# Kernel tuning notes

Hardware: AMD Instinct MI355X
Metric: run time of the kernel (lower is better)

Reference implementation:

```python
import jax, jax.numpy as jnp
import numpy as np

UNITS = 1024
INPUT_DIM = 2048
OUTPUT_DIM = 1000
EPS = 0.01
DT = 0.1
BATCH = 8192


def _kaiming_like(key, shape, fan_in):
    # matches torch kaiming_uniform_(a=sqrt(5)) bound = sqrt(6/((1+5)*fan_in)) = 1/sqrt(fan_in)
    bound = 1.0 / np.sqrt(fan_in)
    return jax.random.uniform(key, shape, jnp.float32, -bound, bound)


def setup_inputs() -> dict:
    key = jax.random.key(0)
    ks = jax.random.split(key, 12)
    x = jax.random.normal(ks[0], (BATCH, INPUT_DIM), jnp.float32)
    W_in = _kaiming_like(ks[1], (UNITS, INPUT_DIM), INPUT_DIM)
    b_in = _kaiming_like(ks[2], (UNITS,), INPUT_DIM)
    W1 = _kaiming_like(ks[3], (UNITS, UNITS), UNITS)
    b1 = _kaiming_like(ks[4], (UNITS,), UNITS)
    W2 = _kaiming_like(ks[5], (UNITS, UNITS), UNITS)
    b2 = _kaiming_like(ks[6], (UNITS,), UNITS)
    W3 = _kaiming_like(ks[7], (UNITS, UNITS), UNITS)
    b3 = _kaiming_like(ks[8], (UNITS,), UNITS)
    W_out = _kaiming_like(ks[9], (OUTPUT_DIM, UNITS), UNITS)
    b_out = _kaiming_like(ks[10], (OUTPUT_DIM,), UNITS)
    return {"x": x, "W_in": W_in, "b_in": b_in, "W1": W1, "b1": b1,
            "W2": W2, "b2": b2, "W3": W3, "b3": b3,
            "W_out": W_out, "b_out": b_out}


def transnet_layer(z, W, b):
    # z: (B, 2U). Implicit layer: A y = rhs, output = C y - rhs (== -y mathematically)
    U = W.shape[0]
    u_in, v_in = z[:, :U], z[:, U:]
    relu_u = jax.nn.relu(u_in)
    rhs_u = u_in + DT * b                      # (B, U)
    rhs_v = v_in + (DT / EPS) * relu_u         # (B, U)
    rhs = jnp.concatenate([rhs_u, rhs_v], axis=1)  # (B, 2U)
    eye = jnp.eye(U, dtype=z.dtype)
    A = jnp.block([[eye, DT * W],
                   [-DT * W.T, (1.0 + DT / EPS) * eye]])  # (2U, 2U), batch-independent
    # factor once, solve against all batch rhs columns at once
    y = jnp.linalg.solve(A, rhs.T).T           # (B, 2U)
    u, v = y[:, :U], y[:, U:]
    u_out = DT * (v @ W.T) - u_in - DT * b
    v_out = -DT * (u @ W) + (DT / EPS) * v - v_in - (DT / EPS) * relu_u
    return jnp.concatenate([u_out, v_out], axis=1)


def reference(x, W_in, b_in, W1, b1, W2, b2, W3, b3, W_out, b_out):
    z = x @ W_in.T + b_in                      # (B, U)
    z = jnp.concatenate([z, jax.nn.relu(z)], axis=1)  # (B, 2U)
    z = transnet_layer(z, W1, b1)
    z = transnet_layer(z, W2, b2)
    z = transnet_layer(z, W3, b3)
    z = z[:, :UNITS]
    logits = jax.nn.softmax(z @ W_out.T + b_out, axis=1)
    return logits
```

## Files before the change

kernel.cpp:

```cpp
#include <hip/hip_runtime.h>
#include <hip/hip_bf16.h>
#include <cstdint>


typedef __bf16 bf16;
typedef __bf16 bf16x4 __attribute__((ext_vector_type(4)));
typedef __bf16 bf16x8 __attribute__((ext_vector_type(8)));
typedef float  f32x4  __attribute__((ext_vector_type(4)));

#define C_DT    0.1f
#define C_DTEPS 10.0f
#define C_DINV  (1.0f/11.0f)
#define C_MSC   (0.01f/121.0f)

__device__ __forceinline__ void async_load16(const bf16* g, bf16* l) {
    __builtin_amdgcn_global_load_lds(
        (__attribute__((address_space(1))) void*)(g),
        (__attribute__((address_space(3))) void*)(l),
        16, 0, 0);
}

__device__ __forceinline__ void remap_block(int& bx, int& by) {
    if (gridDim.y == 64) {
        const int lin  = by * 8 + bx;
        const int xcd  = lin & 7;
        const int slot = lin >> 3;
        by = xcd * 8 + (slot & 7);
        bx = slot >> 3;
    }
}

template<int EPI>
__global__ __launch_bounds__(256, 2)
void gemm_bt(const bf16* __restrict__ A, const bf16* __restrict__ B,
             float* __restrict__ out_f,
             bf16* __restrict__ out_b1, bf16* __restrict__ out_b2,
             const float* __restrict__ e0, const float* __restrict__ e1,
             const float* __restrict__ e2, const bf16* __restrict__ eb,
             int M, int N, int K, float sgn)
{
    __shared__ __attribute__((aligned(16))) char smem[16384];
    bf16* sA = (bf16*)smem;
    bf16* sB = (bf16*)(smem + 8192);

    const int t    = threadIdx.x;
    const int wave = t >> 6;
    const int lane = t & 63;
    int bx = blockIdx.x, by = blockIdx.y;
    remap_block(bx, by);
    const long row0 = (long)by * 128;
    const long col0 = (long)bx * 128;
    const int wr = wave >> 1, wc = wave & 1;

    f32x4 acc[4][4];
#pragma unroll
    for (int i = 0; i < 4; i++)
#pragma unroll
        for (int j = 0; j < 4; j++)
            acc[i][j] = f32x4{0.f, 0.f, 0.f, 0.f};

    const int  q  = t >> 2;
    const int  gp = ((t & 3) + 4 - ((q + (q >> 2)) & 3)) & 3;
    const int  scol = gp * 8;
    const bf16* gA = A + (row0 + q) * (long)K + scol;
    const bf16* gB = B + (col0 + q) * (long)K + scol;
    bf16* lA = sA + wave * 512;
    bf16* lB = sB + wave * 512;

    const int l15  = lane & 15;
    const int fch  = ((lane >> 4) + l15 + (l15 >> 2)) & 3;
    const int aoff = (wr * 64 + l15) * 32 + fch * 8;
    const int boff = (wc * 64 + l15) * 32 + fch * 8;

    for (int k0 = 0; k0 < K; k0 += 32) {
        __syncthreads();
        async_load16(gA + k0,                 lA);
        async_load16(gA + 64 * (long)K + k0,  lA + 2048);
        async_load16(gB + k0,                 lB);
        async_load16(gB + 64 * (long)K + k0,  lB + 2048);
        __syncthreads();

        bf16x8 af[4], bfv[4];
#pragma unroll
        for (int i = 0; i < 4; i++)
            af[i] = *(const bf16x8*)(sA + aoff + i * 16 * 32);
#pragma unroll
        for (int j = 0; j < 4; j++)
            bfv[j] = *(const bf16x8*)(sB + boff + j * 16 * 32);
#pragma unroll
        for (int i = 0; i < 4; i++)
#pragma unroll
            for (int j = 0; j < 4; j++)
                acc[i][j] = __builtin_amdgcn_mfma_f32_16x16x32_bf16(
                    af[i], bfv[j], acc[i][j], 0, 0, 0);
    }

    __syncthreads();
    float* epi = (float*)smem + wave * 1024;
    const int wbase = (lane >> 4) * 256 + (l15 >> 2) * 4 + (l15 & 3);

#pragma unroll
    for (int i = 0; i < 4; i++) {
#pragma unroll
        for (int j = 0; j < 4; j++)
#pragma unroll
            for (int r = 0; r < 4; r++)
                epi[wbase + r * 64 + 16 * j] = acc[i][j][r];

#pragma unroll
        for (int qq = 0; qq < 4; qq++) {
            const f32x4 a4 = ((const f32x4*)epi)[qq * 64 + lane];
            const long m   = row0 + wr * 64 + i * 16 + qq * 4 + (lane >> 4);
            const long n   = col0 + wc * 64 + 4 * l15;
            const long idx = m * (long)N + n;

            if (EPI == 0) {
                const f32x4 b0 = *(const f32x4*)(e0 + n);
                const f32x4 b1 = *(const f32x4*)(e1 + n);
                f32x4 tv; bf16x4 rv, hv;
#pragma unroll
                for (int e = 0; e < 4; e++) {
                    tv[e] = a4[e] + b0[e];
                    rv[e] = (bf16)fmaxf(tv[e], 0.f);
                    hv[e] = (bf16)(tv[e] + C_DT * b1[e]);
                }
                *(f32x4*)(out_f + idx)   = tv;
                *(bf16x4*)(out_b1 + idx) = rv;
                *(bf16x4*)(out_b2 + idx) = hv;
            } else if (EPI == 1) {
                bf16x4 ov;
#pragma unroll
                for (int e = 0; e < 4; e++)
                    ov[e] = (bf16)(((m == n + e) ? C_DINV : 0.f) - C_MSC * a4[e]);
                *(bf16x4*)(out_b1 + idx) = ov;
            } else if (EPI == 2) {
                const f32x4  u0 = *(const f32x4*)(e0 + idx);
                const bf16x4 vv = *(const bf16x4*)(eb + idx);
                bf16x4 ov;
#pragma unroll
                for (int e = 0; e < 4; e++)
                    ov[e] = (bf16)(sgn * (float)vv[e]
                                   + C_DTEPS * fmaxf(u0[e], 0.f) + C_DT * a4[e]);
                *(bf16x4*)(out_b1 + idx) = ov;
            } else if (EPI == 3) {
                bf16x4 ov;
#pragma unroll
                for (int e = 0; e < 4; e++) ov[e] = (bf16)a4[e];
                *(bf16x4*)(out_b1 + idx) = ov;
            } else if (EPI == 4) {
                const f32x4 u0 = *(const f32x4*)(e0 + idx);
                const f32x4 b1 = *(const f32x4*)(e1 + n);
                const f32x4 b2 = *(const f32x4*)(e2 + n);
                f32x4 un; bf16x4 hv;
#pragma unroll
                for (int e = 0; e < 4; e++) {
                    un[e] = C_DT * a4[e] - u0[e] - C_DT * b1[e];
                    hv[e] = (bf16)(un[e] + C_DT * b2[e]);
                }
                *(f32x4*)(out_f + idx)   = un;
                *(bf16x4*)(out_b1 + idx) = hv;
            } else {
                const f32x4 u0 = *(const f32x4*)(e0 + idx);
                const f32x4 b1 = *(const f32x4*)(e1 + n);
                bf16x4 hv, lv;
#pragma unroll
                for (int e = 0; e < 4; e++) {
                    float un = C_DT * a4[e] - u0[e] - C_DT * b1[e];
                    bf16 h = (bf16)un;
                    hv[e] = h;
                    lv[e] = (bf16)(un - (float)h);
                }
                *(bf16x4*)(out_b1 + idx) = hv;
                *(bf16x4*)(out_b2 + idx) = lv;
            }
        }
    }
}

__global__ __launch_bounds__(256, 2)
void gemm_split(const bf16* __restrict__ Ah, const bf16* __restrict__ Al,
                const bf16* __restrict__ Bh, const bf16* __restrict__ Bl,
                float* __restrict__ out, const float* __restrict__ bias,
                int M, int N, int K, int blim)
{
    __shared__ __attribute__((aligned(16))) char smem[32768];
    bf16* sAh = (bf16*)smem;
    bf16* sAl = (bf16*)(smem +  8192);
    bf16* sBh = (bf16*)(smem + 16384);
    bf16* sBl = (bf16*)(smem + 24576);

    const int t    = threadIdx.x;
    const int wave = t >> 6;
    const int lane = t & 63;
    int bx = blockIdx.x, by = blockIdx.y;
    remap_block(bx, by);
    const long row0 = (long)by * 128;
    const long col0 = (long)bx * 128;
    const int wr = wave >> 1, wc = wave & 1;

    f32x4 acc[4][4];
#pragma unroll
    for (int i = 0; i < 4; i++)
#pragma unroll
        for (int j = 0; j < 4; j++)
            acc[i][j] = f32x4{0.f, 0.f, 0.f, 0.f};

    const int  q  = t >> 2;
    const int  gp = ((t & 3) + 4 - ((q + (q >> 2)) & 3)) & 3;
    const int  scol = gp * 8;
    const long gao = (row0 + q) * (long)K + scol;
    const long gbo = (col0 + q) * (long)K + scol;
    const int  lo  = wave * 512;

    const int l15  = lane & 15;
    const int fch  = ((lane >> 4) + l15 + (l15 >> 2)) & 3;
    const int aoff = (wr * 64 + l15) * 32 + fch * 8;
    const int boff = (wc * 64 + l15) * 32 + fch * 8;

    for (int k0 = 0; k0 < K; k0 += 32) {
        __syncthreads();
        async_load16(Ah + gao + k0,                 sAh + lo);
        async_load16(Ah + gao + 64 * (long)K + k0,  sAh + lo + 2048);
        async_load16(Al + gao + k0,                 sAl + lo);
        async_load16(Al + gao + 64 * (long)K + k0,  sAl + lo + 2048);
        async_load16(Bh + gbo + k0,                 sBh + lo);
        async_load16(Bh + gbo + 64 * (long)K + k0,  sBh + lo + 2048);
        async_load16(Bl + gbo + k0,                 sBl + lo);
        async_load16(Bl + gbo + 64 * (long)K + k0,  sBl + lo + 2048);
        __syncthreads();

        bf16x8 ah[4], al[4], bh[4], bl[4];
#pragma unroll
        for (int i = 0; i < 4; i++) {
            ah[i] = *(const bf16x8*)(sAh + aoff + i * 16 * 32);
            al[i] = *(const bf16x8*)(sAl + aoff + i * 16 * 32);
        }
#pragma unroll
        for (int j = 0; j < 4; j++) {
            bh[j] = *(const bf16x8*)(sBh + boff + j * 16 * 32);
            bl[j] = *(const bf16x8*)(sBl + boff + j * 16 * 32);
        }
#pragma unroll
        for (int i = 0; i < 4; i++)
#pragma unroll
            for (int j = 0; j < 4; j++) {
                acc[i][j] = __builtin_amdgcn_mfma_f32_16x16x32_bf16(
                    ah[i], bh[j], acc[i][j], 0, 0, 0);
                acc[i][j] = __builtin_amdgcn_mfma_f32_16x16x32_bf16(
                    ah[i], bl[j], acc[i][j], 0, 0, 0);
                acc[i][j] = __builtin_amdgcn_mfma_f32_16x16x32_bf16(
                    al[i], bh[j], acc[i][j], 0, 0, 0);
            }
    }

    __syncthreads();
    float* epi = (float*)smem + wave * 1024;
    const int wbase = (lane >> 4) * 256 + (l15 >> 2) * 4 + (l15 & 3);

#pragma unroll
    for (int i = 0; i < 4; i++) {
#pragma unroll
        for (int j = 0; j < 4; j++)
#pragma unroll
            for (int r = 0; r < 4; r++)
                epi[wbase + r * 64 + 16 * j] = acc[i][j][r];

#pragma unroll
        for (int qq = 0; qq < 4; qq++) {
            f32x4 a4 = ((const f32x4*)epi)[qq * 64 + lane];
            const long m   = row0 + wr * 64 + i * 16 + qq * 4 + (lane >> 4);
            const long n   = col0 + wc * 64 + 4 * l15;
            f32x4 bv = f32x4{0.f, 0.f, 0.f, 0.f};
            if (n < blim) bv = *(const f32x4*)(bias + n);
#pragma unroll
            for (int e = 0; e < 4; e++) a4[e] += bv[e];
            *(f32x4*)(out + m * (long)N + n) = a4;
        }
    }
}

__global__ void conv_f2b_v4(const float* __restrict__ in, bf16* __restrict__ out)
{
    const long i4 = (long)blockIdx.x * 256 + threadIdx.x;
    const f32x4 v = ((const f32x4*)in)[i4];
    bf16x4 o;
#pragma unroll
    for (int e = 0; e < 4; e++) o[e] = (bf16)v[e];
    ((bf16x4*)out)[i4] = o;
}

__global__ void prep_w(const float* __restrict__ W, bf16* __restrict__ Wb,
                       bf16* __restrict__ Wtb)
{
    __shared__ float tile[32][33];
    const int bx = blockIdx.x * 32, by = blockIdx.y * 32;
    const int tx = threadIdx.x & 31, ty = threadIdx.x >> 5;
#pragma unroll
    for (int i = 0; i < 32; i += 8) {
        float v = W[(long)(by + ty + i) * 1024 + bx + tx];
        tile[ty + i][tx] = v;
        Wb[(long)(by + ty + i) * 1024 + bx + tx] = (bf16)v;
    }
    __syncthreads();
#pragma unroll
    for (int i = 0; i < 32; i += 8)
        Wtb[(long)(bx + ty + i) * 1024 + by + tx] = (bf16)tile[tx][ty + i];
}

__global__ void prep_wout(const float* __restrict__ w, bf16* __restrict__ wh,
                          bf16* __restrict__ wl)
{
    const long i4   = (long)blockIdx.x * 256 + threadIdx.x;
    const long base = i4 * 4;
    const int  nrow = (int)(base >> 10);
    bf16x4 h, l;
    if (nrow < 1000) {
        const f32x4 v = ((const f32x4*)w)[i4];
#pragma unroll
        for (int e = 0; e < 4; e++) {
            bf16 hh = (bf16)v[e];
            h[e] = hh;
            l[e] = (bf16)(v[e] - (float)hh);
        }
    } else {
#pragma unroll
        for (int e = 0; e < 4; e++) { h[e] = (bf16)0.f; l[e] = (bf16)0.f; }
    }
    ((bf16x4*)wh)[i4] = h;
    ((bf16x4*)wl)[i4] = l;
}

__global__ __launch_bounds__(256)
void softmax_rows(const float* __restrict__ logits, float* __restrict__ out)
{
    const int row = blockIdx.x;
    const float* lp = logits + (long)row * 1024;
    const int t = threadIdx.x;
    float v[4];
    float mx = -1e30f;
#pragma unroll
    for (int i = 0; i < 4; i++) {
        const int c = t + i * 256;
        v[i] = (c < 1000) ? lp[c] : -1e30f;
        mx = fmaxf(mx, v[i]);
    }
#pragma unroll
    for (int off = 32; off; off >>= 1)
        mx = fmaxf(mx, __shfl_xor(mx, off));
    __shared__ float sm[4], ss[4];
    const int wave = t >> 6;
    if ((t & 63) == 0) sm[wave] = mx;
    __syncthreads();
    mx = fmaxf(fmaxf(sm[0], sm[1]), fmaxf(sm[2], sm[3]));
    float sum = 0.f;
#pragma unroll
    for (int i = 0; i < 4; i++) {
        v[i] = __expf(v[i] - mx);
        sum += v[i];
    }
#pragma unroll
    for (int off = 32; off; off >>= 1)
        sum += __shfl_xor(sum, off);
    if ((t & 63) == 0) ss[wave] = sum;
    __syncthreads();
    const float inv = 1.f / (ss[0] + ss[1] + ss[2] + ss[3]);
#pragma unroll
    for (int i = 0; i < 4; i++) {
        const int c = t + i * 256;
        if (c < 1000) out[(long)row * 1000 + c] = v[i] * inv;
    }
}

extern "C" void kernel_launch(void* const* d_in, const int* in_sizes, int n_in,
                              void* d_out, int out_size, void* d_ws, size_t ws_size,
                              hipStream_t stream)
{
    const float* x     = (const float*)d_in[0];
    const float* W_in  = (const float*)d_in[1];
    const float* b_in  = (const float*)d_in[2];
    const float* Ws[3] = {(const float*)d_in[3], (const float*)d_in[5], (const float*)d_in[7]};
    const float* bs[3] = {(const float*)d_in[4], (const float*)d_in[6], (const float*)d_in[8]};
    const float* W_out = (const float*)d_in[9];
    const float* b_out = (const float*)d_in[10];
    float* out = (float*)d_out;

    char* ws = (char*)d_ws;
    const size_t MB = 1u << 20;
    bf16*  xb    = (bf16*)(ws);
    bf16*  Winb  = (bf16*)(ws +  32 * MB);
    bf16*  Wouth = (bf16*)(ws +  36 * MB);
    bf16*  Woutl = (bf16*)(ws +  38 * MB);
    bf16*  Wbf   = (bf16*)(ws +  40 * MB);
    bf16*  Wtbf  = (bf16*)(ws +  42 * MB);
    bf16*  Minvb = (bf16*)(ws +  44 * MB);
    float* u_a   = (float*)(ws +  46 * MB);
    float* u_b   = (float*)(ws +  78 * MB);
    bf16*  vb    = (bf16*)(ws + 110 * MB);
    bf16*  rhsub = (bf16*)(ws + 126 * MB);
    bf16*  r_b   = (bf16*)(ws + 142 * MB);
    bf16*  zh    = rhsub;
    bf16*  zl    = r_b;
    float* logits = u_b;

    const dim3 blk(256);
    const dim3 gBig(8, 64);
    const dim3 gSm(8, 8);
    const dim3 gT(32, 32);

    conv_f2b_v4<<<16384, blk, 0, stream>>>(x, xb);
    conv_f2b_v4<<<2048,  blk, 0, stream>>>(W_in, Winb);
    prep_wout<<<1024, blk, 0, stream>>>(W_out, Wouth, Woutl);

    gemm_bt<0><<<gBig, blk, 0, stream>>>(xb, Winb, u_a, vb, rhsub,
                                         b_in, bs[0], nullptr, nullptr,
                                         8192, 1024, 2048, 1.f);

    float* uin[3]  = {u_a, u_b, u_a};
    float* uout[3] = {u_b, u_a, nullptr};
    for (int l = 0; l < 3; l++) {
        prep_w<<<gT, blk, 0, stream>>>(Ws[l], Wbf, Wtbf);
        gemm_bt<1><<<gSm, blk, 0, stream>>>(Wtbf, Wtbf, nullptr, Minvb, nullptr,
                                            nullptr, nullptr, nullptr, nullptr,
                                            1024, 1024, 1024, 1.f);
        gemm_bt<2><<<gBig, blk, 0, stream>>>(rhsub, Wtbf, nullptr, r_b, nullptr,
                                             uin[l], nullptr, nullptr, vb,
                                             8192, 1024, 1024, (l == 0) ? 1.f : -1.f);
        gemm_bt<3><<<gBig, blk, 0, stream>>>(r_b, Minvb, nullptr, vb, nullptr,
                                             nullptr, nullptr, nullptr, nullptr,
                                             8192, 1024, 1024, 1.f);
        if (l < 2) {
            gemm_bt<4><<<gBig, blk, 0, stream>>>(vb, Wbf, uout[l], rhsub, nullptr,
                                                 uin[l], bs[l], bs[l + 1], nullptr,
                                                 8192, 1024, 1024, 1.f);
        } else {
            gemm_bt<5><<<gBig, blk, 0, stream>>>(vb, Wbf, nullptr, zh, zl,
                                                 uin[l], bs[l], nullptr, nullptr,
                                                 8192, 1024, 1024, 1.f);
        }
    }

    gemm_split<<<gBig, blk, 0, stream>>>(zh, zl, Wouth, Woutl, logits, b_out,
                                         8192, 1024, 1024, 1000);
    softmax_rows<<<8192, blk, 0, stream>>>(logits, out);
}
```

Before: 591.3 us.

## Fold per-layer rhs GEMM into weight-side product and double-buffer LDS

Each layer's batch-sized GEMM that built the right-hand side (rhs·W^T) is replaced by a small 1024x1024 product Minv·W computed once per layer. Its result is concatenated with Minv into a [Minv | dt·Minv·W] operand, so a single K=2048 GEMM over a concatenated activation buffer [rhs_u | relu-derived term] produces v directly. This removes one full 8192x1024x1024 GEMM per layer. The epilogues are reworked to write the concatenated activation layout, with new leading-dimension parameters. Both GEMM kernels also get double-buffered LDS staging with one barrier per k-step, which doubles shared memory per block and may reduce occupancy.

Result: slower. 609.2 us (+3.0%).

```diff
diff --git a/kernel.cpp b/kernel.cpp
--- a/kernel.cpp
+++ b/kernel.cpp
@@ -37,11 +37,12 @@
              bf16* __restrict__ out_b1, bf16* __restrict__ out_b2,
              const float* __restrict__ e0, const float* __restrict__ e1,
              const float* __restrict__ e2, const bf16* __restrict__ eb,
-             int M, int N, int K, float sgn)
-{
-    __shared__ __attribute__((aligned(16))) char smem[16384];
-    bf16* sA = (bf16*)smem;
-    bf16* sB = (bf16*)(smem + 8192);
+             int M, int N, int K, int lda, int ldb,
+             int ldf, int ld1, int ld2, float sgn)
+{
+    __shared__ __attribute__((aligned(16))) char smem[32768];
+    bf16* sAe = (bf16*)smem;
+    bf16* sBe = (bf16*)(smem + 16384);
 
     const int t    = threadIdx.x;
     const int wave = t >> 6;
@@ -61,41 +62,47 @@
 
     const int  q  = t >> 2;
     const int  gp = ((t & 3) + 4 - ((q + (q >> 2)) & 3)) & 3;
-    const int  scol = gp * 8;
-    const bf16* gA = A + (row0 + q) * (long)K + scol;
-    const bf16* gB = B + (col0 + q) * (long)K + scol;
-    bf16* lA = sA + wave * 512;
-    bf16* lB = sB + wave * 512;
+    const bf16* gA = A + (row0 + q) * (long)lda + gp * 8;
+    const bf16* gB = B + (col0 + q) * (long)ldb + gp * 8;
 
     const int l15  = lane & 15;
     const int fch  = ((lane >> 4) + l15 + (l15 >> 2)) & 3;
     const int aoff = (wr * 64 + l15) * 32 + fch * 8;
     const int boff = (wc * 64 + l15) * 32 + fch * 8;
 
-    for (int k0 = 0; k0 < K; k0 += 32) {
-        __syncthreads();
-        async_load16(gA + k0,                 lA);
-        async_load16(gA + 64 * (long)K + k0,  lA + 2048);
-        async_load16(gB + k0,                 lB);
-        async_load16(gB + 64 * (long)K + k0,  lB + 2048);
-        __syncthreads();
+    auto stage = [&](int buf, int k0) {
+        bf16* dA = sAe + buf * 4096 + wave * 512;
+        bf16* dB = sBe + buf * 4096 + wave * 512;
+        async_load16(gA + k0,                     dA);
+        async_load16(gA + 64 * (long)lda + k0,    dA + 2048);
+        async_load16(gB + k0,                     dB);
+        async_load16(gB + 64 * (long)ldb + k0,    dB + 2048);
+    };
+
+    const int nIter = K >> 5;
+    stage(0, 0);
+    __syncthreads();
+    for (int k = 0; k < nIter; k++) {
+        const int cur = k & 1;
+        if (k + 1 < nIter) stage(cur ^ 1, (k + 1) << 5);
 
         bf16x8 af[4], bfv[4];
 #pragma unroll
         for (int i = 0; i < 4; i++)
-            af[i] = *(const bf16x8*)(sA + aoff + i * 16 * 32);
+            af[i] = *(const bf16x8*)(sAe + cur * 4096 + aoff + i * 16 * 32);
 #pragma unroll
         for (int j = 0; j < 4; j++)
-            bfv[j] = *(const bf16x8*)(sB + boff + j * 16 * 32);
+            bfv[j] = *(const bf16x8*)(sBe + cur * 4096 + boff + j * 16 * 32);
 #pragma unroll
         for (int i = 0; i < 4; i++)
 #pragma unroll
             for (int j = 0; j < 4; j++)
                 acc[i][j] = __builtin_amdgcn_mfma_f32_16x16x32_bf16(
                     af[i], bfv[j], acc[i][j], 0, 0, 0);
-    }
-
-    __syncthreads();
+
+        __syncthreads();
+    }
+
     float* epi = (float*)smem + wave * 1024;
     const int wbase = (lane >> 4) * 256 + (l15 >> 2) * 4 + (l15 & 3);
 
@@ -110,57 +117,56 @@
 #pragma unroll
         for (int qq = 0; qq < 4; qq++) {
             const f32x4 a4 = ((const f32x4*)epi)[qq * 64 + lane];
-            const long m   = row0 + wr * 64 + i * 16 + qq * 4 + (lane >> 4);
-            const long n   = col0 + wc * 64 + 4 * l15;
-            const long idx = m * (long)N + n;
+            const long m = row0 + wr * 64 + i * 16 + qq * 4 + (lane >> 4);
+            const long n = col0 + wc * 64 + 4 * l15;
 
             if (EPI == 0) {
-                const f32x4 b0 = *(const f32x4*)(e0 + n);
                 const f32x4 b1 = *(const f32x4*)(e1 + n);
+                const f32x4 b2 = *(const f32x4*)(e2 + n);
                 f32x4 tv; bf16x4 rv, hv;
 #pragma unroll
                 for (int e = 0; e < 4; e++) {
-                    tv[e] = a4[e] + b0[e];
-                    rv[e] = (bf16)fmaxf(tv[e], 0.f);
-                    hv[e] = (bf16)(tv[e] + C_DT * b1[e]);
+                    tv[e] = a4[e] + b1[e];
+                    rv[e] = (bf16)(11.f * fmaxf(tv[e], 0.f));
+                    hv[e] = (bf16)(tv[e] + C_DT * b2[e]);
                 }
-                *(f32x4*)(out_f + idx)   = tv;
-                *(bf16x4*)(out_b1 + idx) = rv;
-                *(bf16x4*)(out_b2 + idx) = hv;
+                *(f32x4*)(out_f + m * (long)ldf + n)    = tv;
+                *(bf16x4*)(out_b1 + m * (long)ld1 + n)  = rv;
+                *(bf16x4*)(out_b2 + m * (long)ld2 + n)  = hv;
             } else if (EPI == 1) {
                 bf16x4 ov;
 #pragma unroll
                 for (int e = 0; e < 4; e++)
                     ov[e] = (bf16)(((m == n + e) ? C_DINV : 0.f) - C_MSC * a4[e]);
-                *(bf16x4*)(out_b1 + idx) = ov;
+                *(bf16x4*)(out_b1 + m * (long)ld1 + n) = ov;
+                *(bf16x4*)(out_b2 + m * (long)ld2 + n) = ov;
             } else if (EPI == 2) {
-                const f32x4  u0 = *(const f32x4*)(e0 + idx);
-                const bf16x4 vv = *(const bf16x4*)(eb + idx);
                 bf16x4 ov;
 #pragma unroll
-                for (int e = 0; e < 4; e++)
-                    ov[e] = (bf16)(sgn * (float)vv[e]
-                                   + C_DTEPS * fmaxf(u0[e], 0.f) + C_DT * a4[e]);
-                *(bf16x4*)(out_b1 + idx) = ov;
+                for (int e = 0; e < 4; e++) ov[e] = (bf16)(sgn * a4[e]);
+                *(bf16x4*)(out_b1 + m * (long)ld1 + n) = ov;
             } else if (EPI == 3) {
                 bf16x4 ov;
 #pragma unroll
                 for (int e = 0; e < 4; e++) ov[e] = (bf16)a4[e];
-                *(bf16x4*)(out_b1 + idx) = ov;
+                *(bf16x4*)(out_b1 + m * (long)ld1 + n) = ov;
             } else if (EPI == 4) {
-                const f32x4 u0 = *(const f32x4*)(e0 + idx);
-                const f32x4 b1 = *(const f32x4*)(e1 + n);
-                const f32x4 b2 = *(const f32x4*)(e2 + n);
-                f32x4 un; bf16x4 hv;
+                const f32x4  u0 = *(const f32x4*)(e0 + m * (long)ldf + n);
+                const f32x4  b1 = *(const f32x4*)(e1 + n);
+                const f32x4  b2 = *(const f32x4*)(e2 + n);
+                const bf16x4 vv = *(const bf16x4*)(eb + m * (long)N + n);
+                f32x4 un; bf16x4 rv, hv;
 #pragma unroll
                 for (int e = 0; e < 4; e++) {
                     un[e] = C_DT * a4[e] - u0[e] - C_DT * b1[e];
+                    rv[e] = (bf16)(C_DTEPS * fmaxf(un[e], 0.f) - (float)vv[e]);
                     hv[e] = (bf16)(un[e] + C_DT * b2[e]);
                 }
-                *(f32x4*)(out_f + idx)   = un;
-                *(bf16x4*)(out_b1 + idx) = hv;
+                *(f32x4*)(out_f + m * (long)ldf + n)    = un;
+                *(bf16x4*)(out_b1 + m * (long)ld1 + n)  = rv;
+                *(bf16x4*)(out_b2 + m * (long)ld2 + n)  = hv;
             } else {
-                const f32x4 u0 = *(const f32x4*)(e0 + idx);
+                const f32x4 u0 = *(const f32x4*)(e0 + m * (long)ldf + n);
                 const f32x4 b1 = *(const f32x4*)(e1 + n);
                 bf16x4 hv, lv;
 #pragma unroll
@@ -170,8 +176,8 @@
                     hv[e] = h;
                     lv[e] = (bf16)(un - (float)h);
                 }
-                *(bf16x4*)(out_b1 + idx) = hv;
-                *(bf16x4*)(out_b2 + idx) = lv;
+                *(bf16x4*)(out_b1 + m * (long)ld1 + n) = hv;
+                *(bf16x4*)(out_b2 + m * (long)ld2 + n) = lv;
             }
         }
     }
@@ -183,11 +189,11 @@
                 float* __restrict__ out, const float* __restrict__ bias,
                 int M, int N, int K, int blim)
 {
-    __shared__ __attribute__((aligned(16))) char smem[32768];
+    __shared__ __attribute__((aligned(16))) char smem[65536];
     bf16* sAh = (bf16*)smem;
-    bf16* sAl = (bf16*)(smem +  8192);
-    bf16* sBh = (bf16*)(smem + 16384);
-    bf16* sBl = (bf16*)(smem + 24576);
+    bf16* sAl = (bf16*)(smem + 16384);
+    bf16* sBh = (bf16*)(smem + 32768);
+    bf16* sBl = (bf16*)(smem + 49152);
 
     const int t    = threadIdx.x;
     const int wave = t >> 6;
@@ -207,38 +213,43 @@
 
     const int  q  = t >> 2;
     const int  gp = ((t & 3) + 4 - ((q + (q >> 2)) & 3)) & 3;
-    const int  scol = gp * 8;
-    const long gao = (row0 + q) * (long)K + scol;
-    const long gbo = (col0 + q) * (long)K + scol;
-    const int  lo  = wave * 512;
+    const long gao = (row0 + q) * (long)K + gp * 8;
+    const long gbo = (col0 + q) * (long)K + gp * 8;
 
     const int l15  = lane & 15;
     const int fch  = ((lane >> 4) + l15 + (l15 >> 2)) & 3;
     const int aoff = (wr * 64 + l15) * 32 + fch * 8;
     const int boff = (wc * 64 + l15) * 32 + fch * 8;
 
-    for (int k0 = 0; k0 < K; k0 += 32) {
-        __syncthreads();
-        async_load16(Ah + gao + k0,                 sAh + lo);
-        async_load16(Ah + gao + 64 * (long)K + k0,  sAh + lo + 2048);
-        async_load16(Al + gao + k0,                 sAl + lo);
-        async_load16(Al + gao + 64 * (long)K + k0,  sAl + lo + 2048);
-        async_load16(Bh + gbo + k0,                 sBh + lo);
-        async_load16(Bh + gbo + 64 * (long)K + k0,  sBh + lo + 2048);
-        async_load16(Bl + gbo + k0,                 sBl + lo);
-        async_load16(Bl + gbo + 64 * (long)K + k0,  sBl + lo + 2048);
-        __syncthreads();
+    auto stage = [&](int buf, int k0) {
+        const int d = buf * 4096 + wave * 512;
+        async_load16(Ah + gao + k0,                 sAh + d);
+        async_load16(Ah + gao + 64 * (long)K + k0,  sAh + d + 2048);
+        async_load16(Al + gao + k0,                 sAl + d);
+        async_load16(Al + gao + 64 * (long)K + k0,  sAl + d + 2048);
+        async_load16(Bh + gbo + k0,                 sBh + d);
+        async_load16(Bh + gbo + 64 * (long)K + k0,  sBh + d + 2048);
+        async_load16(Bl + gbo + k0,                 sBl + d);
+        async_load16(Bl + gbo + 64 * (long)K + k0,  sBl + d + 2048);
+    };
+
+    const int nIter = K >> 5;
+    stage(0, 0);
+    __syncthreads();
+    for (int k = 0; k < nIter; k++) {
+        const int cur = k & 1;
+        if (k + 1 < nIter) stage(cur ^ 1, (k + 1) << 5);
 
         bf16x8 ah[4], al[4], bh[4], bl[4];
 #pragma unroll
         for (int i = 0; i < 4; i++) {
-            ah[i] = *(const bf16x8*)(sAh + aoff + i * 16 * 32);
-            al[i] = *(const bf16x8*)(sAl + aoff + i * 16 * 32);
+            ah[i] = *(const bf16x8*)(sAh + cur * 4096 + aoff + i * 16 * 32);
+            al[i] = *(const bf16x8*)(sAl + cur * 4096 + aoff + i * 16 * 32);
         }
 #pragma unroll
         for (int j = 0; j < 4; j++) {
-            bh[j] = *(const bf16x8*)(sBh + boff + j * 16 * 32);
-            bl[j] = *(const bf16x8*)(sBl + boff + j * 16 * 32);
+            bh[j] = *(const bf16x8*)(sBh + cur * 4096 + boff + j * 16 * 32);
+            bl[j] = *(const bf16x8*)(sBl + cur * 4096 + boff + j * 16 * 32);
         }
 #pragma unroll
         for (int i = 0; i < 4; i++)
@@ -251,9 +262,9 @@
                 acc[i][j] = __builtin_amdgcn_mfma_f32_16x16x32_bf16(
                     al[i], bh[j], acc[i][j], 0, 0, 0);
             }
-    }
-
-    __syncthreads();
+        __syncthreads();
+    }
+
     float* epi = (float*)smem + wave * 1024;
     const int wbase = (lane >> 4) * 256 + (l15 >> 2) * 4 + (l15 & 3);
 
@@ -268,8 +279,8 @@
 #pragma unroll
         for (int qq = 0; qq < 4; qq++) {
             f32x4 a4 = ((const f32x4*)epi)[qq * 64 + lane];
-            const long m   = row0 + wr * 64 + i * 16 + qq * 4 + (lane >> 4);
-            const long n   = col0 + wc * 64 + 4 * l15;
+            const long m = row0 + wr * 64 + i * 16 + qq * 4 + (lane >> 4);
+            const long n = col0 + wc * 64 + 4 * l15;
             f32x4 bv = f32x4{0.f, 0.f, 0.f, 0.f};
             if (n < blim) bv = *(const f32x4*)(bias + n);
 #pragma unroll
@@ -393,13 +404,13 @@
     bf16*  Wbf   = (bf16*)(ws +  40 * MB);
     bf16*  Wtbf  = (bf16*)(ws +  42 * MB);
     bf16*  Minvb = (bf16*)(ws +  44 * MB);
-    float* u_a   = (float*)(ws +  46 * MB);
-    float* u_b   = (float*)(ws +  78 * MB);
-    bf16*  vb    = (bf16*)(ws + 110 * MB);
-    bf16*  rhsub = (bf16*)(ws + 126 * MB);
-    bf16*  r_b   = (bf16*)(ws + 142 * MB);
-    bf16*  zh    = rhsub;
-    bf16*  zl    = r_b;
+    bf16*  Bcat  = (bf16*)(ws +  46 * MB);
+    float* u_a   = (float*)(ws +  50 * MB);
+    float* u_b   = (float*)(ws +  82 * MB);
+    bf16*  AC    = (bf16*)(ws + 114 * MB);
+    bf16*  vb    = (bf16*)(ws + 146 * MB);
+    bf16*  zh    = AC;
+    bf16*  zl    = AC + 8192L * 1024;
     float* logits = u_b;
 
     const dim3 blk(256);
@@ -411,31 +422,37 @@
     conv_f2b_v4<<<2048,  blk, 0, stream>>>(W_in, Winb);
     prep_wout<<<1024, blk, 0, stream>>>(W_out, Wouth, Woutl);
 
-    gemm_bt<0><<<gBig, blk, 0, stream>>>(xb, Winb, u_a, vb, rhsub,
-                                         b_in, bs[0], nullptr, nullptr,
-                                         8192, 1024, 2048, 1.f);
+    gemm_bt<0><<<gBig, blk, 0, stream>>>(xb, Winb, u_a, AC, AC + 1024,
+                                         nullptr, b_in, bs[0], nullptr,
+                                         8192, 1024, 2048, 2048, 2048,
+                                         1024, 2048, 2048, 1.f);
 
     float* uin[3]  = {u_a, u_b, u_a};
     float* uout[3] = {u_b, u_a, nullptr};
     for (int l = 0; l < 3; l++) {
         prep_w<<<gT, blk, 0, stream>>>(Ws[l], Wbf, Wtbf);
-        gemm_bt<1><<<gSm, blk, 0, stream>>>(Wtbf, Wtbf, nullptr, Minvb, nullptr,
+        gemm_bt<1><<<gSm, blk, 0, stream>>>(Wtbf, Wtbf, nullptr, Minvb, Bcat,
                                             nullptr, nullptr, nullptr, nullptr,
-                                            1024, 1024, 1024, 1.f);
-        gemm_bt<2><<<gBig, blk, 0, stream>>>(rhsub, Wtbf, nullptr, r_b, nullptr,
-                                             uin[l], nullptr, nullptr, vb,
-                                             8192, 1024, 1024, (l == 0) ? 1.f : -1.f);
-        gemm_bt<3><<<gBig, blk, 0, stream>>>(r_b, Minvb, nullptr, vb, nullptr,
+                                            1024, 1024, 1024, 1024, 1024,
+                                            0, 1024, 2048, 1.f);
+        gemm_bt<2><<<gSm, blk, 0, stream>>>(Minvb, Wbf, nullptr, Bcat + 1024, nullptr,
+                                            nullptr, nullptr, nullptr, nullptr,
+                                            1024, 1024, 1024, 1024, 1024,
+                                            0, 2048, 0, C_DT);
+        gemm_bt<3><<<gBig, blk, 0, stream>>>(AC, Bcat, nullptr, vb, nullptr,
                                              nullptr, nullptr, nullptr, nullptr,
-                                             8192, 1024, 1024, 1.f);
+                                             8192, 1024, 2048, 2048, 2048,
+                                             0, 1024, 0, 1.f);
         if (l < 2) {
-            gemm_bt<4><<<gBig, blk, 0, stream>>>(vb, Wbf, uout[l], rhsub, nullptr,
-                                                 uin[l], bs[l], bs[l + 1], nullptr,
-                                                 8192, 1024, 1024, 1.f);
+            gemm_bt<4><<<gBig, blk, 0, stream>>>(vb, Wbf, uout[l], AC, AC + 1024,
+                                                 uin[l], bs[l], bs[l + 1], vb,
+                                                 8192, 1024, 1024, 1024, 1024,
+                                                 1024, 2048, 2048, 1.f);
         } else {
             gemm_bt<5><<<gBig, blk, 0, stream>>>(vb, Wbf, nullptr, zh, zl,
                                                  uin[l], bs[l], nullptr, nullptr,
-                                                 8192, 1024, 1024, 1.f);
+                                                 8192, 1024, 1024, 1024, 1024,
+                                                 1024, 1024, 1024, 1.f);
         }
     }
 
```
